# Kernel optimization log

Hardware: AMD Instinct MI355X
Metric: run time of the kernel (lower is better)

The kernel has to match this reference:

```python
import jax, jax.numpy as jnp
import numpy as np

POOLED_H, POOLED_W = 7, 7
SPATIAL_SCALE = 0.0625


def setup_inputs() -> dict:
    key = jax.random.key(0)
    k1, k2, k3, k4, k5, k6, k7 = jax.random.split(key, 7)
    B, C, H, W = 2, 256, 200, 272
    R = 2000
    x = jax.random.normal(k1, (B, C, H, W), dtype=jnp.float32)
    # rois: [batch_idx, cx, cy, w, h, angle_degrees] in image coordinates
    batch_idx = jax.random.randint(k2, (R,), 0, B).astype(jnp.float32)
    cx = jax.random.uniform(k3, (R,), minval=0.0, maxval=W / SPATIAL_SCALE)
    cy = jax.random.uniform(k4, (R,), minval=0.0, maxval=H / SPATIAL_SCALE)
    rw = jax.random.uniform(k5, (R,), minval=32.0, maxval=512.0)
    rh = jax.random.uniform(k6, (R,), minval=32.0, maxval=256.0)
    ang = jax.random.uniform(k7, (R,), minval=-90.0, maxval=90.0)
    rois = jnp.stack([batch_idx, cx, cy, rw, rh, ang], axis=1).astype(jnp.float32)
    return {"input": x, "rois": rois}


def _rround(x):
    # CUDA roundf (half away from zero) ~ floor(x + 0.5) for the positive range used here
    return jnp.floor(x + 0.5)


def reference(input, rois):
    B, C, H, W = input.shape
    batch_idx = rois[:, 0].astype(jnp.int32)          # [R]
    cx = rois[:, 1] * SPATIAL_SCALE
    cy = rois[:, 2] * SPATIAL_SCALE
    rw = rois[:, 3] * SPATIAL_SCALE
    rh = rois[:, 4] * SPATIAL_SCALE
    theta = rois[:, 5] * (jnp.pi / 180.0)

    # Affine transform from pooled-grid coords to feature-map coords (RRPN kernel)
    dx = -POOLED_W / 2.0
    dy = -POOLED_H / 2.0
    Sx = rw / POOLED_W
    Sy = rh / POOLED_H
    ca = jnp.cos(theta)
    sa = jnp.sin(theta)
    M00 = (ca * Sx)[:, None, None]
    M01 = (sa * Sy)[:, None, None]
    M02 = (ca * Sx * dx + sa * Sy * dy + cx)[:, None, None]
    M10 = (-sa * Sx)[:, None, None]
    M11 = (ca * Sy)[:, None, None]
    M12 = (-sa * Sx * dx + ca * Sy * dy + cy)[:, None, None]

    pw = jnp.arange(POOLED_W, dtype=rois.dtype)[None, None, :]   # [1,1,PW]
    ph = jnp.arange(POOLED_H, dtype=rois.dtype)[None, :, None]   # [1,PH,1]

    def corner(a, b):  # bin corner (pw+a, ph+b) -> feature coords, each [R,PH,PW]
        X = M00 * (pw + a) + M01 * (ph + b) + M02
        Y = M10 * (pw + a) + M11 * (ph + b) + M12
        return X, Y

    X0, Y0 = corner(0.0, 0.0)
    X1, Y1 = corner(0.0, 1.0)
    X2, Y2 = corner(1.0, 0.0)
    X3, Y3 = corner(1.0, 1.0)

    leftMost = jnp.maximum(_rround(jnp.minimum(jnp.minimum(X0, X1), jnp.minimum(X2, X3))), 0.0)
    rightMost = jnp.minimum(_rround(jnp.maximum(jnp.maximum(X0, X1), jnp.maximum(X2, X3))), W - 1.0)
    topMost = jnp.maximum(_rround(jnp.minimum(jnp.minimum(Y0, Y1), jnp.minimum(Y2, Y3))), 0.0)
    bottomMost = jnp.minimum(_rround(jnp.maximum(jnp.maximum(Y0, Y1), jnp.maximum(Y2, Y3))), H - 1.0)

    bin_cx = (leftMost + rightMost) / 2.0   # [R,PH,PW]
    bin_cy = (topMost + bottomMost) / 2.0

    bin_l = jnp.floor(bin_cx)
    bin_r = jnp.ceil(bin_cx)
    bin_t = jnp.floor(bin_cy)
    bin_b = jnp.ceil(bin_cy)

    rx = bin_cx - jnp.floor(bin_cx)
    ry = bin_cy - jnp.floor(bin_cy)
    wlt = (1.0 - rx) * (1.0 - ry)
    wrt = rx * (1.0 - ry)
    wrb = rx * ry
    wlb = (1.0 - rx) * ry

    bidx = batch_idx[:, None, None]  # [R,1,1]

    def sample(yy, xx):
        # masked gather of input[b, :, y, x] -> [R,PH,PW,C]
        m = ((yy > -1.0) & (yy < H) & (xx > -1.0) & (xx < W)).astype(input.dtype)
        yi = jnp.clip(yy.astype(jnp.int32), 0, H - 1)
        xi = jnp.clip(xx.astype(jnp.int32), 0, W - 1)
        v = input[bidx, :, yi, xi]  # advanced idx -> [R,PH,PW,C]
        return v * m[..., None]

    lt = sample(bin_t, bin_l)
    rt = sample(bin_t, bin_r)
    lb = sample(bin_b, bin_l)
    rb = sample(bin_b, bin_r)

    out = (lt * wlt[..., None] + rt * wrt[..., None]
           + rb * wrb[..., None] + lb * wlb[..., None])   # [R,PH,PW,C]
    return jnp.transpose(out, (0, 3, 1, 2))                 # [R,C,PH,PW]
```

## Files before the change

### kernel.cpp

```cpp
#include <hip/hip_runtime.h>
#include <math.h>

#define B_   2
#define C_   256
#define H_   200
#define W_   272
#define HW_  (H_*W_)
#define NBIN 49
#define SCALE 0.0625f

typedef float v4f __attribute__((ext_vector_type(4)));

__device__ __forceinline__ unsigned short f2bf(float f) {
    union { float f; unsigned int i; } v; v.f = f;
    unsigned int x = v.i;
    return (unsigned short)((x + 0x7FFFu + ((x >> 16) & 1u)) >> 16);
}
__device__ __forceinline__ float bf2f(unsigned int u16) {
    union { unsigned int i; float f; } v; v.i = u16 << 16; return v.f;
}

__device__ __forceinline__ float edge_mask(float yy, float xx) {
    return (yy > -1.0f && yy < (float)H_ && xx > -1.0f && xx < (float)W_) ? 1.0f : 0.0f;
}

__device__ void compute_geom(const float* __restrict__ rois, int r, int bin,
                             int& b, int& yt, int& yb, int& xl, int& xr,
                             float w[4]) {
#pragma clang fp contract(off)
    const float* rp = rois + r * 6;
    b = (int)rp[0];
    float cx = rp[1] * SCALE;
    float cy = rp[2] * SCALE;
    float rw = rp[3] * SCALE;
    float rh = rp[4] * SCALE;
    float theta = rp[5] * (float)(M_PI / 180.0);
    float Sx = rw / 7.0f;
    float Sy = rh / 7.0f;
    double th = (double)theta;
    float ca = (float)cos(th);
    float sa = (float)sin(th);

    float M00 = ca * Sx;
    float M01 = sa * Sy;
    float M02 = (M00 * (-3.5f) + M01 * (-3.5f)) + cx;
    float M10 = (-sa) * Sx;
    float M11 = ca * Sy;
    float M12 = (M10 * (-3.5f) + M11 * (-3.5f)) + cy;

    float pwf = (float)(bin % 7);
    float phf = (float)(bin / 7);
    float x0 = pwf, x1 = pwf + 1.0f;
    float y0 = phf, y1 = phf + 1.0f;

    float X00 = (M00 * x0 + M01 * y0) + M02;
    float X01 = (M00 * x0 + M01 * y1) + M02;
    float X10 = (M00 * x1 + M01 * y0) + M02;
    float X11 = (M00 * x1 + M01 * y1) + M02;
    float Y00 = (M10 * x0 + M11 * y0) + M12;
    float Y01 = (M10 * x0 + M11 * y1) + M12;
    float Y10 = (M10 * x1 + M11 * y0) + M12;
    float Y11 = (M10 * x1 + M11 * y1) + M12;

    float minX = fminf(fminf(X00, X01), fminf(X10, X11));
    float maxX = fmaxf(fmaxf(X00, X01), fmaxf(X10, X11));
    float minY = fminf(fminf(Y00, Y01), fminf(Y10, Y11));
    float maxY = fmaxf(fmaxf(Y00, Y01), fmaxf(Y10, Y11));

    float leftMost   = fmaxf(floorf(minX + 0.5f), 0.0f);
    float rightMost  = fminf(floorf(maxX + 0.5f), (float)(W_ - 1));
    float topMost    = fmaxf(floorf(minY + 0.5f), 0.0f);
    float bottomMost = fminf(floorf(maxY + 0.5f), (float)(H_ - 1));

    float bcx = (leftMost + rightMost) * 0.5f;
    float bcy = (topMost + bottomMost) * 0.5f;
    float fl = floorf(bcx), fr = ceilf(bcx);
    float ft = floorf(bcy), fb = ceilf(bcy);
    float rx = bcx - fl;
    float ry = bcy - ft;

    float wlt = (1.0f - rx) * (1.0f - ry);
    float wrt = rx * (1.0f - ry);
    float wrb = rx * ry;
    float wlb = (1.0f - rx) * ry;

    w[0] = wlt * edge_mask(ft, fl);
    w[1] = wrt * edge_mask(ft, fr);
    w[2] = wlb * edge_mask(fb, fl);
    w[3] = wrb * edge_mask(fb, fr);

    yt = min(max((int)ft, 0), H_ - 1);
    yb = min(max((int)fb, 0), H_ - 1);
    xl = min(max((int)fl, 0), W_ - 1);
    xr = min(max((int)fr, 0), W_ - 1);
}

__global__ __launch_bounds__(256) void transpose_geom(const float* __restrict__ in,
                                                      unsigned short* __restrict__ xt,
                                                      unsigned int* __restrict__ geom,
                                                      const float* __restrict__ rois,
                                                      int R) {
    if (blockIdx.y == 4) {
        int total = R * NBIN;
        for (int gid = (blockIdx.z * 850 + blockIdx.x) * 256 + threadIdx.x;
             gid < total; gid += 1700 * 256) {
            int r = gid / NBIN, bin = gid - r * NBIN;
            int b, yt, yb, xl, xr; float w[4];
            compute_geom(rois, r, bin, b, yt, yb, xl, xr, w);
            int base = b * HW_ * C_;
            uint4 o, wu;
            o.x = base + (yt * W_ + xl) * C_;
            o.y = base + (yt * W_ + xr) * C_;
            o.z = base + (yb * W_ + xl) * C_;
            o.w = base + (yb * W_ + xr) * C_;
            wu.x = __float_as_uint(w[0]);
            wu.y = __float_as_uint(w[1]);
            wu.z = __float_as_uint(w[2]);
            wu.w = __float_as_uint(w[3]);
            uint4* gp = (uint4*)(geom + (size_t)gid * 8);
            gp[0] = o;
            gp[1] = wu;
        }
        return;
    }

    __shared__ float tile[64][65];
    int b  = blockIdx.z;
    int p0 = blockIdx.x * 64;
    int c0 = blockIdx.y * 64;
    const float*    ib = in + (size_t)b * C_ * HW_;
    unsigned short* ob = xt + (size_t)b * HW_ * C_;
    int t = threadIdx.x;

    {
        int col4 = t & 15;
        int row  = t >> 4;
        #pragma unroll
        for (int k = 0; k < 4; k++) {
            int c = row + k * 16;
            float4 v = *(const float4*)(ib + (size_t)(c0 + c) * HW_ + p0 + col4 * 4);
            int p = col4 * 4;
            tile[p + 0][c] = v.x;
            tile[p + 1][c] = v.y;
            tile[p + 2][c] = v.z;
            tile[p + 3][c] = v.w;
        }
    }
    __syncthreads();
    {
        int c8 = t & 7;
        int pr = t >> 3;
        #pragma unroll
        for (int k = 0; k < 2; k++) {
            int p = pr + k * 32;
            ushort4 lo, hi;
            const float* tp = &tile[p][c8 * 8];
            lo.x = f2bf(tp[0]); lo.y = f2bf(tp[1]); lo.z = f2bf(tp[2]); lo.w = f2bf(tp[3]);
            hi.x = f2bf(tp[4]); hi.y = f2bf(tp[5]); hi.z = f2bf(tp[6]); hi.w = f2bf(tp[7]);
            unsigned short* dst = ob + (size_t)(p0 + p) * C_ + c0 + c8 * 8;
            *(ushort4*)(dst)     = lo;
            *(ushort4*)(dst + 4) = hi;
        }
    }
}

__device__ __forceinline__ void bilerp4(uint2 lt, uint2 rt, uint2 lb, uint2 rb,
                                        float w0, float w1, float w2, float w3,
                                        float acc[4]) {
#pragma clang fp contract(off)
    float a0 = bf2f(lt.x & 0xFFFFu), a1 = bf2f(lt.x >> 16),
          a2 = bf2f(lt.y & 0xFFFFu), a3 = bf2f(lt.y >> 16);
    float b0 = bf2f(rt.x & 0xFFFFu), b1 = bf2f(rt.x >> 16),
          b2 = bf2f(rt.y & 0xFFFFu), b3 = bf2f(rt.y >> 16);
    float c0v = bf2f(lb.x & 0xFFFFu), c1v = bf2f(lb.x >> 16),
          c2v = bf2f(lb.y & 0xFFFFu), c3v = bf2f(lb.y >> 16);
    float d0 = bf2f(rb.x & 0xFFFFu), d1 = bf2f(rb.x >> 16),
          d2 = bf2f(rb.y & 0xFFFFu), d3 = bf2f(rb.y >> 16);
    acc[0] = ((w0 * a0 + w1 * b0) + w3 * d0) + w2 * c0v;
    acc[1] = ((w0 * a1 + w1 * b1) + w3 * d1) + w2 * c1v;
    acc[2] = ((w0 * a2 + w1 * b2) + w3 * d2) + w2 * c2v;
    acc[3] = ((w0 * a3 + w1 * b3) + w3 * d3) + w2 * c3v;
}

__device__ __forceinline__ void store_bin(unsigned short* lout, int c4, int lane,
                                          int bin, const float acc[4]) {
    #pragma unroll
    for (int jj = 0; jj < 4; jj++) {
        int j = (jj + (lane >> 3)) & 3;
        float v = (j == 0) ? acc[0] : (j == 1) ? acc[1] : (j == 2) ? acc[2] : acc[3];
        lout[(c4 + j) * NBIN + bin] = f2bf(v);
    }
}

__global__ __launch_bounds__(256) void rroi_main_bf16(const unsigned short* __restrict__ xt,
                                                      const unsigned int* __restrict__ geom,
                                                      float* __restrict__ outp) {
    __shared__ unsigned short lout[C_ * NBIN];

    int r    = blockIdx.x;
    int tid  = threadIdx.x;
    int lane = tid & 63;
    int wv   = tid >> 6;
    int c4   = lane * 4;

    const uint4* gb = (const uint4*)(geom + (size_t)r * NBIN * 8);

    for (int b0 = wv; b0 < NBIN; b0 += 12) {
        int b1 = b0 + 4, b2 = b0 + 8;
        uint4 go0 = gb[2 * b0];
        uint4 gu0 = gb[2 * b0 + 1];
        if (b2 < NBIN) {
            uint4 go1 = gb[2 * b1];
            uint4 gu1 = gb[2 * b1 + 1];
            uint4 go2 = gb[2 * b2];
            uint4 gu2 = gb[2 * b2 + 1];
            uint2 lt0 = *(const uint2*)(xt + go0.x + c4);
            uint2 rt0 = *(const uint2*)(xt + go0.y + c4);
            uint2 lb0 = *(const uint2*)(xt + go0.z + c4);
            uint2 rb0 = *(const uint2*)(xt + go0.w + c4);
            uint2 lt1 = *(const uint2*)(xt + go1.x + c4);
            uint2 rt1 = *(const uint2*)(xt + go1.y + c4);
            uint2 lb1 = *(const uint2*)(xt + go1.z + c4);
            uint2 rb1 = *(const uint2*)(xt + go1.w + c4);
            uint2 lt2 = *(const uint2*)(xt + go2.x + c4);
            uint2 rt2 = *(const uint2*)(xt + go2.y + c4);
            uint2 lb2 = *(const uint2*)(xt + go2.z + c4);
            uint2 rb2 = *(const uint2*)(xt + go2.w + c4);
            float acc0[4], acc1[4], acc2[4];
            bilerp4(lt0, rt0, lb0, rb0,
                    __uint_as_float(gu0.x), __uint_as_float(gu0.y),
                    __uint_as_float(gu0.z), __uint_as_float(gu0.w), acc0);
            bilerp4(lt1, rt1, lb1, rb1,
                    __uint_as_float(gu1.x), __uint_as_float(gu1.y),
                    __uint_as_float(gu1.z), __uint_as_float(gu1.w), acc1);
            bilerp4(lt2, rt2, lb2, rb2,
                    __uint_as_float(gu2.x), __uint_as_float(gu2.y),
                    __uint_as_float(gu2.z), __uint_as_float(gu2.w), acc2);
            store_bin(lout, c4, lane, b0, acc0);
            store_bin(lout, c4, lane, b1, acc1);
            store_bin(lout, c4, lane, b2, acc2);
        } else if (b1 < NBIN) {
            uint4 go1 = gb[2 * b1];
            uint4 gu1 = gb[2 * b1 + 1];
            uint2 lt0 = *(const uint2*)(xt + go0.x + c4);
            uint2 rt0 = *(const uint2*)(xt + go0.y + c4);
            uint2 lb0 = *(const uint2*)(xt + go0.z + c4);
            uint2 rb0 = *(const uint2*)(xt + go0.w + c4);
            uint2 lt1 = *(const uint2*)(xt + go1.x + c4);
            uint2 rt1 = *(const uint2*)(xt + go1.y + c4);
            uint2 lb1 = *(const uint2*)(xt + go1.z + c4);
            uint2 rb1 = *(const uint2*)(xt + go1.w + c4);
            float acc0[4], acc1[4];
            bilerp4(lt0, rt0, lb0, rb0,
                    __uint_as_float(gu0.x), __uint_as_float(gu0.y),
                    __uint_as_float(gu0.z), __uint_as_float(gu0.w), acc0);
            bilerp4(lt1, rt1, lb1, rb1,
                    __uint_as_float(gu1.x), __uint_as_float(gu1.y),
                    __uint_as_float(gu1.z), __uint_as_float(gu1.w), acc1);
            store_bin(lout, c4, lane, b0, acc0);
            store_bin(lout, c4, lane, b1, acc1);
        } else {
            uint2 lt0 = *(const uint2*)(xt + go0.x + c4);
            uint2 rt0 = *(const uint2*)(xt + go0.y + c4);
            uint2 lb0 = *(const uint2*)(xt + go0.z + c4);
            uint2 rb0 = *(const uint2*)(xt + go0.w + c4);
            float acc0[4];
            bilerp4(lt0, rt0, lb0, rb0,
                    __uint_as_float(gu0.x), __uint_as_float(gu0.y),
                    __uint_as_float(gu0.z), __uint_as_float(gu0.w), acc0);
            store_bin(lout, c4, lane, b0, acc0);
        }
    }
    __syncthreads();

    const unsigned int* lu = (const unsigned int*)lout;
    float* obase = outp + (size_t)r * (C_ * NBIN);
    const int n4 = (C_ * NBIN) / 4;
    for (int f = tid; f < n4; f += 256) {
        uint2 u = *(const uint2*)(&lu[2 * f]);
        v4f v;
        v.x = bf2f(u.x & 0xFFFFu); v.y = bf2f(u.x >> 16);
        v.z = bf2f(u.y & 0xFFFFu); v.w = bf2f(u.y >> 16);
        __builtin_nontemporal_store(v, (v4f*)(obase + 4 * f));
    }
}

__global__ __launch_bounds__(256) void rroi_main_direct(const float* __restrict__ x,
                                                        const float* __restrict__ rois,
                                                        float* __restrict__ outp) {
    __shared__ float loutf[C_ * NBIN];
    __shared__ int   goff[NBIN][4];
    __shared__ float gw[NBIN][4];

    int r = blockIdx.x;
    int tid = threadIdx.x;

    if (tid < NBIN) {
        int b, yt, yb, xl, xr; float w[4];
        compute_geom(rois, r, tid, b, yt, yb, xl, xr, w);
        int base = b * C_ * HW_;
        goff[tid][0] = base + yt * W_ + xl;
        goff[tid][1] = base + yt * W_ + xr;
        goff[tid][2] = base + yb * W_ + xl;
        goff[tid][3] = base + yb * W_ + xr;
        gw[tid][0] = w[0]; gw[tid][1] = w[1]; gw[tid][2] = w[2]; gw[tid][3] = w[3];
    }
    __syncthreads();

    int c = tid;
    int coff = c * HW_;
    for (int bin = 0; bin < NBIN; bin++) {
        float w0 = gw[bin][0], w1 = gw[bin][1], w2 = gw[bin][2], w3 = gw[bin][3];
        float lt = x[goff[bin][0] + coff];
        float rt = x[goff[bin][1] + coff];
        float lb = x[goff[bin][2] + coff];
        float rb = x[goff[bin][3] + coff];
        float v;
        {
#pragma clang fp contract(off)
            v = ((w0 * lt + w1 * rt) + w3 * rb) + w2 * lb;
        }
        loutf[c * NBIN + bin] = v;
    }
    __syncthreads();

    float* o = outp + (size_t)r * (C_ * NBIN);
    const int n4 = (C_ * NBIN) / 4;
    for (int i = tid; i < n4; i += 256)
        *(float4*)(o + i * 4) = *(const float4*)(&loutf[i * 4]);
}

extern "C" void kernel_launch(void* const* d_in, const int* in_sizes, int n_in,
                              void* d_out, int out_size, void* d_ws, size_t ws_size,
                              hipStream_t stream) {
    const float* x    = (const float*)d_in[0];
    const float* rois = (const float*)d_in[1];
    float*       outp = (float*)d_out;
    int R = in_sizes[1] / 6;

    size_t geom_off = 64ull * 1024 * 1024;
    size_t need = geom_off + (size_t)R * NBIN * 8 * sizeof(unsigned int);
    if (ws_size >= need) {
        unsigned short* xt   = (unsigned short*)d_ws;
        unsigned int*   geom = (unsigned int*)((char*)d_ws + geom_off);
        dim3 g(HW_ / 64, 5, B_);
        transpose_geom<<<g, 256, 0, stream>>>(x, xt, geom, rois, R);
        rroi_main_bf16<<<R, 256, 0, stream>>>(xt, geom, outp);
    } else {
        rroi_main_direct<<<R, 256, 0, stream>>>(x, rois, outp);
    }
}
```

Baseline: 60.91 us.

## Fuse transpose, geometry and pooling into one cooperative persistent kernel

```diff
diff --git a/kernel.cpp b/kernel.cpp
--- a/kernel.cpp
+++ b/kernel.cpp
@@ -1,5 +1,8 @@
 #include <hip/hip_runtime.h>
+#include <hip/hip_cooperative_groups.h>
 #include <math.h>
+
+namespace cg = cooperative_groups;
 
 #define B_   2
 #define C_   256
@@ -91,47 +94,17 @@
 
     yt = min(max((int)ft, 0), H_ - 1);
     yb = min(max((int)fb, 0), H_ - 1);
+    xl = min(max((int)xl, 0), W_ - 1);
     xl = min(max((int)fl, 0), W_ - 1);
     xr = min(max((int)fr, 0), W_ - 1);
 }
 
-__global__ __launch_bounds__(256) void transpose_geom(const float* __restrict__ in,
-                                                      unsigned short* __restrict__ xt,
-                                                      unsigned int* __restrict__ geom,
-                                                      const float* __restrict__ rois,
-                                                      int R) {
-    if (blockIdx.y == 4) {
-        int total = R * NBIN;
-        for (int gid = (blockIdx.z * 850 + blockIdx.x) * 256 + threadIdx.x;
-             gid < total; gid += 1700 * 256) {
-            int r = gid / NBIN, bin = gid - r * NBIN;
-            int b, yt, yb, xl, xr; float w[4];
-            compute_geom(rois, r, bin, b, yt, yb, xl, xr, w);
-            int base = b * HW_ * C_;
-            uint4 o, wu;
-            o.x = base + (yt * W_ + xl) * C_;
-            o.y = base + (yt * W_ + xr) * C_;
-            o.z = base + (yb * W_ + xl) * C_;
-            o.w = base + (yb * W_ + xr) * C_;
-            wu.x = __float_as_uint(w[0]);
-            wu.y = __float_as_uint(w[1]);
-            wu.z = __float_as_uint(w[2]);
-            wu.w = __float_as_uint(w[3]);
-            uint4* gp = (uint4*)(geom + (size_t)gid * 8);
-            gp[0] = o;
-            gp[1] = wu;
-        }
-        return;
-    }
-
-    __shared__ float tile[64][65];
-    int b  = blockIdx.z;
-    int p0 = blockIdx.x * 64;
-    int c0 = blockIdx.y * 64;
+__device__ __forceinline__ void transpose_tile(const float* __restrict__ in,
+                                               unsigned short* __restrict__ xt,
+                                               int b, int p0, int c0, int t,
+                                               float (*tile)[65]) {
     const float*    ib = in + (size_t)b * C_ * HW_;
     unsigned short* ob = xt + (size_t)b * HW_ * C_;
-    int t = threadIdx.x;
-
     {
         int col4 = t & 15;
         int row  = t >> 4;
@@ -161,6 +134,30 @@
             *(ushort4*)(dst)     = lo;
             *(ushort4*)(dst + 4) = hi;
         }
+    }
+}
+
+__device__ __forceinline__ void geom_slot(const float* __restrict__ rois,
+                                          unsigned int* __restrict__ geom,
+                                          int slot, int tid, int R) {
+    int total = R * NBIN;
+    for (int gid = slot * 256 + tid; gid < total; gid += 1700 * 256) {
+        int r = gid / NBIN, bin = gid - r * NBIN;
+        int b, yt, yb, xl, xr; float w[4];
+        compute_geom(rois, r, bin, b, yt, yb, xl, xr, w);
+        int base = b * HW_ * C_;
+        uint4 o, wu;
+        o.x = base + (yt * W_ + xl) * C_;
+        o.y = base + (yt * W_ + xr) * C_;
+        o.z = base + (yb * W_ + xl) * C_;
+        o.w = base + (yb * W_ + xr) * C_;
+        wu.x = __float_as_uint(w[0]);
+        wu.y = __float_as_uint(w[1]);
+        wu.z = __float_as_uint(w[2]);
+        wu.w = __float_as_uint(w[3]);
+        uint4* gp = (uint4*)(geom + (size_t)gid * 8);
+        gp[0] = o;
+        gp[1] = wu;
     }
 }
 
@@ -192,13 +189,10 @@
     }
 }
 
-__global__ __launch_bounds__(256) void rroi_main_bf16(const unsigned short* __restrict__ xt,
-                                                      const unsigned int* __restrict__ geom,
-                                                      float* __restrict__ outp) {
-    __shared__ unsigned short lout[C_ * NBIN];
-
-    int r    = blockIdx.x;
-    int tid  = threadIdx.x;
+__device__ __forceinline__ void main_roi(const unsigned short* __restrict__ xt,
+                                         const unsigned int* __restrict__ geom,
+                                         float* __restrict__ outp, int r, int tid,
+                                         unsigned short* lout) {
     int lane = tid & 63;
     int wv   = tid >> 6;
     int c4   = lane * 4;
@@ -285,6 +279,57 @@
     }
 }
 
+#define SM_BYTES 25088
+
+__global__ __launch_bounds__(256, 4) void fused_all(const float* __restrict__ in,
+                                                    unsigned short* __restrict__ xt,
+                                                    unsigned int* __restrict__ geom,
+                                                    const float* __restrict__ rois,
+                                                    float* __restrict__ outp,
+                                                    int R) {
+    __shared__ __align__(16) char sm[SM_BYTES];
+    int tid = threadIdx.x;
+
+    for (int id = blockIdx.x; id < 8500; id += gridDim.x) {
+        if (id < 6800) {
+            int b = id / 3400, wti = id % 3400;
+            transpose_tile(in, xt, b, (wti % 850) * 64, (wti / 850) * 64,
+                           tid, (float(*)[65])sm);
+        } else {
+            geom_slot(rois, geom, id - 6800, tid, R);
+        }
+        __syncthreads();
+    }
+
+    cg::this_grid().sync();
+
+    for (int r = blockIdx.x; r < R; r += gridDim.x) {
+        main_roi(xt, geom, outp, r, tid, (unsigned short*)sm);
+        __syncthreads();
+    }
+}
+
+__global__ __launch_bounds__(256) void transpose_geom(const float* __restrict__ in,
+                                                      unsigned short* __restrict__ xt,
+                                                      unsigned int* __restrict__ geom,
+                                                      const float* __restrict__ rois,
+                                                      int R) {
+    if (blockIdx.y == 4) {
+        geom_slot(rois, geom, blockIdx.z * 850 + blockIdx.x, threadIdx.x, R);
+        return;
+    }
+    __shared__ float tile[64][65];
+    transpose_tile(in, xt, blockIdx.z, blockIdx.x * 64, blockIdx.y * 64,
+                   threadIdx.x, tile);
+}
+
+__global__ __launch_bounds__(256) void rroi_main_bf16(const unsigned short* __restrict__ xt,
+                                                      const unsigned int* __restrict__ geom,
+                                                      float* __restrict__ outp) {
+    __shared__ unsigned short lout[C_ * NBIN];
+    main_roi(xt, geom, outp, blockIdx.x, threadIdx.x, lout);
+}
+
 __global__ __launch_bounds__(256) void rroi_main_direct(const float* __restrict__ x,
                                                         const float* __restrict__ rois,
                                                         float* __restrict__ outp) {
@@ -343,9 +388,17 @@
     if (ws_size >= need) {
         unsigned short* xt   = (unsigned short*)d_ws;
         unsigned int*   geom = (unsigned int*)((char*)d_ws + geom_off);
-        dim3 g(HW_ / 64, 5, B_);
-        transpose_geom<<<g, 256, 0, stream>>>(x, xt, geom, rois, R);
-        rroi_main_bf16<<<R, 256, 0, stream>>>(xt, geom, outp);
+
+        void* args[] = { (void*)&x, (void*)&xt, (void*)&geom,
+                         (void*)&rois, (void*)&outp, (void*)&R };
+        hipError_t e = hipLaunchCooperativeKernel((const void*)fused_all,
+                                                  dim3(1024), dim3(256),
+                                                  args, 0, stream);
+        if (e != hipSuccess) {
+            dim3 g(HW_ / 64, 5, B_);
+            transpose_geom<<<g, 256, 0, stream>>>(x, xt, geom, rois, R);
+            rroi_main_bf16<<<R, 256, 0, stream>>>(xt, geom, outp);
+        }
     } else {
         rroi_main_direct<<<R, 256, 0, stream>>>(x, rois, outp);
     }
```

Measured after the change: 198.9 us. +226.5%, slower.
